# Kernel tuning notes

Hardware: AMD Instinct MI355X
Metric: run time of the kernel (lower is better)

## Reference

```python
import jax, jax.numpy as jnp
import numpy as np

N = 10000
E = 160000
NEG_SLOPE = 0.2
BN_EPS = 1e-5


def _gat_conv(x, W, a_src, a_dst, b, src, dst, n, heads):
    # PyG GATConv, concat=False (mean over heads), shared lin for src/dst.
    H = heads
    C = W.shape[1] // H
    h = (x @ W).reshape(n, H, C)                       # (N,H,C)
    e_s = jnp.einsum('nhc,hc->nh', h, a_src)           # (N,H)
    e_d = jnp.einsum('nhc,hc->nh', h, a_dst)
    alpha = jax.nn.leaky_relu(e_s[src] + e_d[dst], NEG_SLOPE)   # (E',H)
    amax = jax.ops.segment_max(alpha, dst, num_segments=n)       # per-dst softmax
    ex = jnp.exp(alpha - amax[dst])
    denom = jax.ops.segment_sum(ex, dst, num_segments=n)
    w = ex / (denom[dst] + 1e-16)
    out = jax.ops.segment_sum(h[src] * w[:, :, None], dst, num_segments=n)  # (N,H,C)
    return out.mean(axis=1) + b


def _bn(x, g, b):
    mu = x.mean(axis=0)
    var = x.var(axis=0)  # biased, as torch BN training forward
    return (x - mu) * jax.lax.rsqrt(var + BN_EPS) * g + b


def setup_inputs() -> dict:
    key = jax.random.key(0)
    ks = jax.random.split(key, 32)
    d = {}
    d['x'] = jax.random.normal(ks[0], (N, 64), jnp.float32)
    d['edge_index'] = jax.random.randint(ks[1], (2, E), 0, N, jnp.int64)
    s = lambda k, shape, fan: jax.random.normal(k, shape, jnp.float32) * (1.0 / np.sqrt(fan))
    d['Wp'] = s(ks[2], (64, 128), 64); d['bp'] = jnp.zeros((128,), jnp.float32)
    # conv0: 8 heads, per-head 128
    d['W0'] = s(ks[3], (128, 8 * 128), 128); d['as0'] = s(ks[4], (8, 128), 128)
    d['ad0'] = s(ks[5], (8, 128), 128); d['b0'] = jnp.zeros((128,), jnp.float32)
    d['g0'] = jnp.ones((128,), jnp.float32); d['be0'] = jnp.zeros((128,), jnp.float32)
    # conv1: same shape
    d['W1'] = s(ks[6], (128, 8 * 128), 128); d['as1'] = s(ks[7], (8, 128), 128)
    d['ad1'] = s(ks[8], (8, 128), 128); d['b1'] = jnp.zeros((128,), jnp.float32)
    d['g1'] = jnp.ones((128,), jnp.float32); d['be1'] = jnp.zeros((128,), jnp.float32)
    # conv2: 1 head, out 64
    d['W2'] = s(ks[9], (128, 64), 128); d['as2'] = s(ks[10], (1, 64), 64)
    d['ad2'] = s(ks[11], (1, 64), 64); d['b2'] = jnp.zeros((64,), jnp.float32)
    d['g2'] = jnp.ones((64,), jnp.float32); d['be2'] = jnp.zeros((64,), jnp.float32)
    # residual projection for layer 2 (128 -> 64)
    d['Wr'] = s(ks[12], (128, 64), 128); d['br'] = jnp.zeros((64,), jnp.float32)
    return d


def reference(x, edge_index, Wp, bp, W0, as0, ad0, b0, g0, be0,
              W1, as1, ad1, b1, g1, be1, W2, as2, ad2, b2, g2, be2, Wr, br):
    n = x.shape[0]
    loops = jnp.arange(n, dtype=edge_index.dtype)
    src = jnp.concatenate([edge_index[0], loops])  # add_self_loops=True
    dst = jnp.concatenate([edge_index[1], loops])
    h = x @ Wp + bp
    # layer 0 (8 heads, identity residual)
    hr = h
    h = jax.nn.elu(_bn(_gat_conv(h, W0, as0, ad0, b0, src, dst, n, 8), g0, be0)) + hr
    # layer 1
    hr = h
    h = jax.nn.elu(_bn(_gat_conv(h, W1, as1, ad1, b1, src, dst, n, 8), g1, be1)) + hr
    # layer 2 (1 head, linear residual 128->64)
    hr = h @ Wr + br
    h = jax.nn.elu(_bn(_gat_conv(h, W2, as2, ad2, b2, src, dst, n, 1), g2, be2)) + hr
    return h
```

## Files before the change

### kernel.cpp

```cpp
#include <hip/hip_runtime.h>
#include <hip/hip_bf16.h>
#include <cstdint>
#include <cstddef>

#define TPB 256

typedef __attribute__((ext_vector_type(8))) short bf16x8;
typedef __attribute__((ext_vector_type(4))) float f32x4;

static __device__ __forceinline__ float bf2f(unsigned short u) {
  union { unsigned int i; float f; } c;
  c.i = ((unsigned int)u) << 16;
  return c.f;
}

__global__ void detect_kernel(const unsigned int* __restrict__ w, int* __restrict__ flag) {
  __shared__ int any32;
  if (threadIdx.x == 0) any32 = 0;
  __syncthreads();
  for (int i = threadIdx.x; i < 1024; i += TPB)
    if (w[2 * i + 1] != 0u) any32 = 1;
  __syncthreads();
  if (threadIdx.x == 0) *flag = any32;
}

__global__ void decode_kernel(const void* __restrict__ raw, const int* __restrict__ flag,
                              int* __restrict__ src, int* __restrict__ dst, int E, int n) {
  int i = blockIdx.x * TPB + threadIdx.x;
  int tot = E + n;
  if (i >= tot) return;
  if (i < E) {
    if (*flag) {
      const int* p = (const int*)raw;
      src[i] = p[i];
      dst[i] = p[E + i];
    } else {
      const long long* p = (const long long*)raw;
      src[i] = (int)p[i];
      dst[i] = (int)p[E + i];
    }
  } else {
    src[i] = i - E;
    dst[i] = i - E;
  }
}

__global__ void count_kernel(const int* __restrict__ dst, int* __restrict__ counts, int etot) {
  int i = blockIdx.x * TPB + threadIdx.x;
  if (i < etot) atomicAdd(&counts[dst[i]], 1);
}

__global__ void scan_kernel(const int* __restrict__ counts, int* __restrict__ row_ptr, int n) {
  __shared__ int part[TPB];
  int tid = threadIdx.x;
  int chunk = (n + TPB - 1) / TPB;
  int begin = tid * chunk;
  int end = begin + chunk; if (end > n) end = n;
  int s = 0;
  for (int i = begin; i < end && i < n; i++) s += counts[i];
  part[tid] = s;
  __syncthreads();
  for (int off = 1; off < TPB; off <<= 1) {
    int v = (tid >= off) ? part[tid - off] : 0;
    __syncthreads();
    part[tid] += v;
    __syncthreads();
  }
  int base = (tid == 0) ? 0 : part[tid - 1];
  for (int i = begin; i < end && i < n; i++) { row_ptr[i] = base; base += counts[i]; }
  if (tid == TPB - 1) row_ptr[n] = base;
}

__global__ void fill_kernel(const int* __restrict__ src, const int* __restrict__ dst,
                            const int* __restrict__ row_ptr, int* __restrict__ fill,
                            int* __restrict__ sorted_src, int etot) {
  int i = blockIdx.x * TPB + threadIdx.x;
  if (i >= etot) return;
  int d = dst[i];
  int pos = row_ptr[d] + atomicAdd(&fill[d], 1);
  sorted_src[pos] = src[i];
}

__global__ void f32_to_bf16_kernel(const float* __restrict__ in, __hip_bfloat16* __restrict__ out, int n) {
  int i = blockIdx.x * TPB + threadIdx.x;
  if (i < n) out[i] = __float2bfloat16(in[i]);
}

__global__ __launch_bounds__(256) void gemm_bf16_kernel(
    const short* __restrict__ A, const short* __restrict__ B,
    const float* __restrict__ bias, float* __restrict__ C,
    __hip_bfloat16* __restrict__ Cb, int M, int N, int K) {
  __shared__ short As[64][40];
  __shared__ short Bs[64][40];

  const int tid = threadIdx.x;
  const int lane = tid & 63;
  const int w = tid >> 6;
  const int bm = blockIdx.x * 64;
  const int bn = blockIdx.y * 64;

  f32x4 acc[4];
#pragma unroll
  for (int nt = 0; nt < 4; nt++) acc[nt] = (f32x4){0.f, 0.f, 0.f, 0.f};

  const int arow = tid >> 2;
  const int akk = (tid & 3) << 3;
  const int bc = tid & 63;
  const int bkg = (tid >> 6) << 3;

  for (int k0 = 0; k0 < K; k0 += 32) {
    {
      int gr = bm + arow;
      if (gr < M) {
        *(bf16x8*)&As[arow][akk] = *(const bf16x8*)&A[(size_t)gr * K + k0 + akk];
      } else {
        bf16x8 z = {0, 0, 0, 0, 0, 0, 0, 0};
        *(bf16x8*)&As[arow][akk] = z;
      }
    }
    {
      bf16x8 t;
#pragma unroll
      for (int j = 0; j < 8; j++)
        t[j] = B[(size_t)(k0 + bkg + j) * N + bn + bc];
      *(bf16x8*)&Bs[bc][bkg] = t;
    }
    __syncthreads();

    bf16x8 a = *(const bf16x8*)&As[w * 16 + (lane & 15)][(lane >> 4) * 8];
#pragma unroll
    for (int nt = 0; nt < 4; nt++) {
      bf16x8 b = *(const bf16x8*)&Bs[nt * 16 + (lane & 15)][(lane >> 4) * 8];
      acc[nt] = __builtin_amdgcn_mfma_f32_16x16x32_bf16(a, b, acc[nt], 0, 0, 0);
    }
    __syncthreads();
  }

#pragma unroll
  for (int nt = 0; nt < 4; nt++) {
    int gc = bn + nt * 16 + (lane & 15);
    float bv = bias ? bias[gc] : 0.f;
#pragma unroll
    for (int q = 0; q < 4; q++) {
      int gr = bm + w * 16 + (lane >> 4) * 4 + q;
      if (gr < M) {
        float val = acc[nt][q] + bv;
        if (C) C[(size_t)gr * N + gc] = val;
        if (Cb) Cb[(size_t)gr * N + gc] = __float2bfloat16(val);
      }
    }
  }
}

__global__ void attn_coeff8_kernel(const unsigned short* __restrict__ gb,
                                   const float* __restrict__ asrc,
                                   const float* __restrict__ adst,
                                   float* __restrict__ es, float* __restrict__ ed) {
  const int v = blockIdx.x;
  const int tid = threadIdx.x;
  ushort4 gu = *(const ushort4*)&gb[(size_t)v * 1024 + 4 * tid];
  float4 av = *(const float4*)&asrc[4 * tid];
  float4 dv = *(const float4*)&adst[4 * tid];
  float gx = bf2f(gu.x), gy = bf2f(gu.y), gz = bf2f(gu.z), gw = bf2f(gu.w);
  float p1 = gx * av.x + gy * av.y + gz * av.z + gw * av.w;
  float p2 = gx * dv.x + gy * dv.y + gz * dv.z + gw * dv.w;
#pragma unroll
  for (int off = 16; off > 0; off >>= 1) {
    p1 += __shfl_down(p1, off);
    p2 += __shfl_down(p2, off);
  }
  if ((tid & 31) == 0) {
    es[(size_t)v * 8 + (tid >> 5)] = p1;
    ed[(size_t)v * 8 + (tid >> 5)] = p2;
  }
}

template <int H, int C>
__global__ void attn_coeff_kernel(const float* __restrict__ g,
                                  const float* __restrict__ asrc,
                                  const float* __restrict__ adst,
                                  float* __restrict__ es, float* __restrict__ ed) {
  int v = blockIdx.x;
  int tid = threadIdx.x;
  __shared__ float rs[2], rd[2];
  const float* grow = g + (size_t)v * (H * C);
  for (int h = 0; h < H; ++h) {
    float gv = grow[h * C + tid];
    float p1 = gv * asrc[h * C + tid];
    float p2 = gv * adst[h * C + tid];
#pragma unroll
    for (int off = 32; off > 0; off >>= 1) {
      p1 += __shfl_down(p1, off);
      p2 += __shfl_down(p2, off);
    }
    if ((tid & 63) == 0) { rs[tid >> 6] = p1; rd[tid >> 6] = p2; }
    __syncthreads();
    if (tid == 0) {
      float s1 = rs[0], s2 = rd[0];
      if (C > 64) { s1 += rs[1]; s2 += rd[1]; }
      es[(size_t)v * H + h] = s1;
      ed[(size_t)v * H + h] = s2;
    }
    __syncthreads();
  }
}

__global__ __launch_bounds__(256) void gat_aggregate8_kernel(
    const int* __restrict__ row_ptr, const int* __restrict__ srcs,
    const unsigned short* __restrict__ gb, const float* __restrict__ es,
    const float* __restrict__ ed, const float* __restrict__ bias,
    float* __restrict__ out) {
  constexpr int T = 256, H = 8, HC = 1024, CHUNK = 64;
  const int v = blockIdx.x;
  const int tid = threadIdx.x;
  const int h = tid & 7;
  const int grp = tid >> 3;
  const int hh = tid >> 5;

  __shared__ float red[T];
  __shared__ float mh[H], invd[H], edv[H];
  __shared__ float wlds[CHUNK * H];
  __shared__ int slds[CHUNK];
  __shared__ float4 red4[T];

  const int begin = row_ptr[v];
  const int deg = row_ptr[v + 1] - begin;

  if (tid < H) edv[tid] = ed[(size_t)v * H + tid];
  __syncthreads();

  float pm = -1e30f;
  for (int j = grp; j < deg; j += 32) {
    int s = srcs[begin + j];
    float a = es[(size_t)s * H + h] + edv[h];
    a = a > 0.f ? a : 0.2f * a;
    pm = fmaxf(pm, a);
  }
  red[tid] = pm;
  __syncthreads();
  if (tid < H) {
    float m = -1e30f;
    for (int gg = 0; gg < 32; gg++) m = fmaxf(m, red[gg * H + tid]);
    mh[tid] = m;
  }
  __syncthreads();

  float ps = 0.f;
  for (int j = grp; j < deg; j += 32) {
    int s = srcs[begin + j];
    float a = es[(size_t)s * H + h] + edv[h];
    a = a > 0.f ? a : 0.2f * a;
    ps += expf(a - mh[h]);
  }
  red[tid] = ps;
  __syncthreads();
  if (tid < H) {
    float d = 0.f;
    for (int gg = 0; gg < 32; gg++) d += red[gg * H + tid];
    invd[tid] = 1.0f / (d + 1e-16f);
  }

  float4 acc = make_float4(0.f, 0.f, 0.f, 0.f);
  for (int base = 0; base < deg; base += CHUNK) {
    int cnt = deg - base; if (cnt > CHUNK) cnt = CHUNK;
    __syncthreads();
    for (int idx = tid; idx < cnt * H; idx += T) {
      int j = idx >> 3, hx = idx & 7;
      int s = srcs[begin + base + j];
      if (hx == 0) slds[j] = s;
      float a = es[(size_t)s * H + hx] + edv[hx];
      a = a > 0.f ? a : 0.2f * a;
      wlds[idx] = expf(a - mh[hx]) * invd[hx];
    }
    __syncthreads();
    int j = 0;
    for (; j + 2 <= cnt; j += 2) {
      int s0 = slds[j], s1 = slds[j + 1];
      float w0 = wlds[j * 8 + hh], w1 = wlds[(j + 1) * 8 + hh];
      ushort4 u0 = *(const ushort4*)&gb[(size_t)s0 * HC + 4 * tid];
      ushort4 u1 = *(const ushort4*)&gb[(size_t)s1 * HC + 4 * tid];
      acc.x += w0 * bf2f(u0.x); acc.y += w0 * bf2f(u0.y);
      acc.z += w0 * bf2f(u0.z); acc.w += w0 * bf2f(u0.w);
      acc.x += w1 * bf2f(u1.x); acc.y += w1 * bf2f(u1.y);
      acc.z += w1 * bf2f(u1.z); acc.w += w1 * bf2f(u1.w);
    }
    if (j < cnt) {
      int s0 = slds[j];
      float w0 = wlds[j * 8 + hh];
      ushort4 u0 = *(const ushort4*)&gb[(size_t)s0 * HC + 4 * tid];
      acc.x += w0 * bf2f(u0.x); acc.y += w0 * bf2f(u0.y);
      acc.z += w0 * bf2f(u0.z); acc.w += w0 * bf2f(u0.w);
    }
  }

  __syncthreads();
  red4[tid] = acc;
  __syncthreads();
  if (tid < 32) {
    float4 s = red4[tid];
#pragma unroll
    for (int hx = 1; hx < 8; hx++) {
      float4 t = red4[tid + 32 * hx];
      s.x += t.x; s.y += t.y; s.z += t.z; s.w += t.w;
    }
    int c0 = 4 * tid;
    out[(size_t)v * 128 + c0 + 0] = s.x * 0.125f + bias[c0 + 0];
    out[(size_t)v * 128 + c0 + 1] = s.y * 0.125f + bias[c0 + 1];
    out[(size_t)v * 128 + c0 + 2] = s.z * 0.125f + bias[c0 + 2];
    out[(size_t)v * 128 + c0 + 3] = s.w * 0.125f + bias[c0 + 3];
  }
}

__global__ __launch_bounds__(256) void gat_aggregate1_kernel(
    const int* __restrict__ row_ptr, const int* __restrict__ srcs,
    const float* __restrict__ g, const float* __restrict__ es,
    const float* __restrict__ ed, const float* __restrict__ bias,
    float* __restrict__ out, int n) {
  const int wave = threadIdx.x >> 6;
  const int lane = threadIdx.x & 63;
  const int v = blockIdx.x * 4 + wave;
  if (v >= n) return;

  const int begin = row_ptr[v];
  const int deg = row_ptr[v + 1] - begin;
  const float edv = ed[v];

  float pm = -1e30f;
  for (int j = lane; j < deg; j += 64) {
    float a = es[srcs[begin + j]] + edv;
    a = a > 0.f ? a : 0.2f * a;
    pm = fmaxf(pm, a);
  }
#pragma unroll
  for (int off = 32; off > 0; off >>= 1) pm = fmaxf(pm, __shfl_xor(pm, off));

  float ps = 0.f;
  for (int j = lane; j < deg; j += 64) {
    float a = es[srcs[begin + j]] + edv;
    a = a > 0.f ? a : 0.2f * a;
    ps += expf(a - pm);
  }
#pragma unroll
  for (int off = 32; off > 0; off >>= 1) ps += __shfl_xor(ps, off);
  const float invd = 1.0f / (ps + 1e-16f);

  float acc = 0.f;
  for (int base = 0; base < deg; base += 64) {
    int cnt = deg - base; if (cnt > 64) cnt = 64;
    int sv = 0; float wv = 0.f;
    if (lane < cnt) {
      sv = srcs[begin + base + lane];
      float a = es[sv] + edv;
      a = a > 0.f ? a : 0.2f * a;
      wv = expf(a - pm) * invd;
    }
    for (int j = 0; j < cnt; j++) {
      int s = __shfl(sv, j);
      float wgt = __shfl(wv, j);
      acc += wgt * g[(size_t)s * 64 + lane];
    }
  }
  out[(size_t)v * 64 + lane] = acc + bias[lane];
}

template <int C>
__global__ void bn_stats_kernel(const float* __restrict__ x, int n, float* __restrict__ sums) {
  constexpr int T = 256;
  constexpr int RPI = T / C;
  constexpr int ITER = 64;
  constexpr int ROWS = RPI * ITER;
  int c = threadIdx.x % C;
  int r0 = threadIdx.x / C;
  int rowBase = blockIdx.x * ROWS;
  float s = 0.f, q = 0.f;
  for (int it = 0; it < ITER; ++it) {
    int r = rowBase + it * RPI + r0;
    if (r < n) {
      float v = x[(size_t)r * C + c];
      s += v; q += v * v;
    }
  }
  __shared__ float ls[T], lq[T];
  ls[threadIdx.x] = s; lq[threadIdx.x] = q;
  __syncthreads();
  if (threadIdx.x < C) {
    float ts = 0.f, tq = 0.f;
    for (int r = 0; r < RPI; ++r) { ts += ls[c + r * C]; tq += lq[c + r * C]; }
    atomicAdd(&sums[c], ts);
    atomicAdd(&sums[C + c], tq);
  }
}

template <int C>
__global__ void bn_elu_res_kernel(const float* __restrict__ x, const float* __restrict__ sums,
                                  const float* __restrict__ gamma, const float* __restrict__ beta,
                                  const float* __restrict__ res, float* __restrict__ out,
                                  __hip_bfloat16* __restrict__ outb, int n) {
  int i = blockIdx.x * TPB + threadIdx.x;
  if (i >= n * C) return;
  int c = i % C;
  float inv_n = 1.0f / (float)n;
  float mu = sums[c] * inv_n;
  float var = sums[C + c] * inv_n - mu * mu;
  float y = (x[i] - mu) * rsqrtf(var + 1e-5f) * gamma[c] + beta[c];
  y = y > 0.f ? y : expm1f(y);
  y += res[i];
  out[i] = y;
  if (outb) outb[i] = __float2bfloat16(y);
}

extern "C" void kernel_launch(void* const* d_in, const int* in_sizes, int n_in,
                              void* d_out, int out_size, void* d_ws, size_t ws_size,
                              hipStream_t stream) {
  const float* x   = (const float*)d_in[0];
  const void*  ei  = d_in[1];
  const float* Wp  = (const float*)d_in[2];
  const float* bp  = (const float*)d_in[3];
  const float* W0  = (const float*)d_in[4];
  const float* as0 = (const float*)d_in[5];
  const float* ad0 = (const float*)d_in[6];
  const float* b0  = (const float*)d_in[7];
  const float* g0  = (const float*)d_in[8];
  const float* be0 = (const float*)d_in[9];
  const float* W1  = (const float*)d_in[10];
  const float* as1 = (const float*)d_in[11];
  const float* ad1 = (const float*)d_in[12];
  const float* b1  = (const float*)d_in[13];
  const float* g1  = (const float*)d_in[14];
  const float* be1 = (const float*)d_in[15];
  const float* W2  = (const float*)d_in[16];
  const float* as2 = (const float*)d_in[17];
  const float* ad2 = (const float*)d_in[18];
  const float* b2  = (const float*)d_in[19];
  const float* g2  = (const float*)d_in[20];
  const float* be2 = (const float*)d_in[21];
  const float* Wr  = (const float*)d_in[22];
  const float* br  = (const float*)d_in[23];

  const int N = in_sizes[0] / 64;
  const int E = in_sizes[1] / 2;
  const int ETOT = E + N;

  char* wsp = (char*)d_ws;
  size_t off = 0;
  auto alloc = [&](size_t bytes) -> void* {
    void* p = wsp + off;
    off += (bytes + 255) & ~(size_t)255;
    return p;
  };
  int*   flag    = (int*)alloc(4);
  int*   e_src   = (int*)alloc((size_t)ETOT * 4);
  int*   e_dst   = (int*)alloc((size_t)ETOT * 4);
  int*   counts  = (int*)alloc((size_t)N * 4);
  int*   fillc   = (int*)alloc((size_t)N * 4);
  int*   row_ptr = (int*)alloc((size_t)(N + 1) * 4);
  int*   s_src   = (int*)alloc((size_t)ETOT * 4);
  float* hA      = (float*)alloc((size_t)N * 128 * 4);
  float* hB      = (float*)alloc((size_t)N * 128 * 4);
  float* gbuf    = (float*)alloc((size_t)N * 64 * 4);
  float* gat     = (float*)alloc((size_t)N * 128 * 4);
  float* es      = (float*)alloc((size_t)N * 8 * 4);
  float* ed      = (float*)alloc((size_t)N * 8 * 4);
  float* bnsum   = (float*)alloc(2 * 128 * 4);
  __hip_bfloat16* gbufb = (__hip_bfloat16*)alloc((size_t)N * 1024 * 2);
  __hip_bfloat16* xb  = (__hip_bfloat16*)alloc((size_t)N * 64 * 2);
  __hip_bfloat16* hAb = (__hip_bfloat16*)alloc((size_t)N * 128 * 2);
  __hip_bfloat16* hBb = (__hip_bfloat16*)alloc((size_t)N * 128 * 2);
  __hip_bfloat16* Wpb = (__hip_bfloat16*)alloc((size_t)64 * 128 * 2);
  __hip_bfloat16* W0b = (__hip_bfloat16*)alloc((size_t)128 * 1024 * 2);
  __hip_bfloat16* W1b = (__hip_bfloat16*)alloc((size_t)128 * 1024 * 2);
  __hip_bfloat16* W2b = (__hip_bfloat16*)alloc((size_t)128 * 64 * 2);
  __hip_bfloat16* Wrb = (__hip_bfloat16*)alloc((size_t)128 * 64 * 2);

  const int egrid = (ETOT + TPB - 1) / TPB;
  const int mgrid = (N + 63) / 64;
  auto cgrid = [](int n) { return (n + TPB - 1) / TPB; };

  detect_kernel<<<1, TPB, 0, stream>>>((const unsigned int*)ei, flag);
  decode_kernel<<<egrid, TPB, 0, stream>>>(ei, flag, e_src, e_dst, E, N);
  hipMemsetAsync(counts, 0, (size_t)N * 4, stream);
  hipMemsetAsync(fillc, 0, (size_t)N * 4, stream);
  count_kernel<<<egrid, TPB, 0, stream>>>(e_dst, counts, ETOT);
  scan_kernel<<<1, TPB, 0, stream>>>(counts, row_ptr, N);
  fill_kernel<<<egrid, TPB, 0, stream>>>(e_src, e_dst, row_ptr, fillc, s_src, ETOT);

  f32_to_bf16_kernel<<<cgrid(N * 64), TPB, 0, stream>>>(x, xb, N * 64);
  f32_to_bf16_kernel<<<cgrid(64 * 128), TPB, 0, stream>>>(Wp, Wpb, 64 * 128);
  f32_to_bf16_kernel<<<cgrid(128 * 1024), TPB, 0, stream>>>(W0, W0b, 128 * 1024);
  f32_to_bf16_kernel<<<cgrid(128 * 1024), TPB, 0, stream>>>(W1, W1b, 128 * 1024);
  f32_to_bf16_kernel<<<cgrid(128 * 64), TPB, 0, stream>>>(W2, W2b, 128 * 64);
  f32_to_bf16_kernel<<<cgrid(128 * 64), TPB, 0, stream>>>(Wr, Wrb, 128 * 64);

  gemm_bf16_kernel<<<dim3(mgrid, 2), 256, 0, stream>>>(
      (const short*)xb, (const short*)Wpb, bp, hA, hAb, N, 128, 64);

  gemm_bf16_kernel<<<dim3(mgrid, 16), 256, 0, stream>>>(
      (const short*)hAb, (const short*)W0b, nullptr, nullptr, gbufb, N, 1024, 128);
  attn_coeff8_kernel<<<N, 256, 0, stream>>>((const unsigned short*)gbufb, as0, ad0, es, ed);
  gat_aggregate8_kernel<<<N, 256, 0, stream>>>(row_ptr, s_src, (const unsigned short*)gbufb, es, ed, b0, gat);
  hipMemsetAsync(bnsum, 0, 2 * 128 * 4, stream);
  bn_stats_kernel<128><<<(N + 127) / 128, 256, 0, stream>>>(gat, N, bnsum);
  bn_elu_res_kernel<128><<<cgrid(N * 128), TPB, 0, stream>>>(gat, bnsum, g0, be0, hA, hB, hBb, N);

  gemm_bf16_kernel<<<dim3(mgrid, 16), 256, 0, stream>>>(
      (const short*)hBb, (const short*)W1b, nullptr, nullptr, gbufb, N, 1024, 128);
  attn_coeff8_kernel<<<N, 256, 0, stream>>>((const unsigned short*)gbufb, as1, ad1, es, ed);
  gat_aggregate8_kernel<<<N, 256, 0, stream>>>(row_ptr, s_src, (const unsigned short*)gbufb, es, ed, b1, gat);
  hipMemsetAsync(bnsum, 0, 2 * 128 * 4, stream);
  bn_stats_kernel<128><<<(N + 127) / 128, 256, 0, stream>>>(gat, N, bnsum);
  bn_elu_res_kernel<128><<<cgrid(N * 128), TPB, 0, stream>>>(gat, bnsum, g1, be1, hB, hA, hAb, N);

  gemm_bf16_kernel<<<dim3(mgrid, 1), 256, 0, stream>>>(
      (const short*)hAb, (const short*)Wrb, br, hB, nullptr, N, 64, 128);
  gemm_bf16_kernel<<<dim3(mgrid, 1), 256, 0, stream>>>(
      (const short*)hAb, (const short*)W2b, nullptr, gbuf, nullptr, N, 64, 128);
  attn_coeff_kernel<1, 64><<<N, 64, 0, stream>>>(gbuf, as2, ad2, es, ed);
  gat_aggregate1_kernel<<<(N + 3) / 4, 256, 0, stream>>>(row_ptr, s_src, gbuf, es, ed, b2, gat, N);
  hipMemsetAsync(bnsum, 0, 2 * 64 * 4, stream);
  bn_stats_kernel<64><<<(N + 255) / 256, 256, 0, stream>>>(gat, N, bnsum);
  bn_elu_res_kernel<64><<<cgrid(N * 64), TPB, 0, stream>>>(gat, bnsum, g2, be2, hB, (float*)d_out, nullptr, N);
}
```

Before: 334.4 us.

## Pre-transpose weights for vectorized GEMM B loads and restructure GAT aggregation

Weights are converted to transposed bf16 once, so the GEMM can load B tiles with 16-byte vector reads instead of strided scalar gathers. The GEMM tile widens to 128 output columns. The 8-head aggregation now caches leaky-relu logits in shared memory for nodes with degree up to 128, so neighbor es values are not re-gathered three times. It also gathers 8 bf16 per thread, unrolled over four neighbors split across two half-blocks. This adds shared memory use and a larger final reduction, and it swaps expf for __expf.

```diff
diff --git a/kernel.cpp b/kernel.cpp
--- a/kernel.cpp
+++ b/kernel.cpp
@@ -6,7 +6,9 @@
 #define TPB 256
 
 typedef __attribute__((ext_vector_type(8))) short bf16x8;
+typedef __attribute__((ext_vector_type(8))) unsigned short ushort8;
 typedef __attribute__((ext_vector_type(4))) float f32x4;
+typedef __attribute__((ext_vector_type(8))) float f32x8;
 
 static __device__ __forceinline__ float bf2f(unsigned short u) {
   union { unsigned int i; float f; } c;
@@ -86,27 +88,43 @@
   if (i < n) out[i] = __float2bfloat16(in[i]);
 }
 
-__global__ __launch_bounds__(256) void gemm_bf16_kernel(
-    const short* __restrict__ A, const short* __restrict__ B,
+__global__ void f32_to_bf16_T_kernel(const float* __restrict__ in, __hip_bfloat16* __restrict__ out,
+                                     int K, int N) {
+  __shared__ float tile[32][33];
+  const int k0 = blockIdx.x * 32, n0 = blockIdx.y * 32;
+  const int tx = threadIdx.x & 31, ty = threadIdx.x >> 5;
+  for (int r = ty; r < 32; r += 8) {
+    int k = k0 + r, n = n0 + tx;
+    tile[r][tx] = (k < K && n < N) ? in[(size_t)k * N + n] : 0.f;
+  }
+  __syncthreads();
+  for (int r = ty; r < 32; r += 8) {
+    int n = n0 + r, k = k0 + tx;
+    if (n < N && k < K) out[(size_t)n * K + k] = __float2bfloat16(tile[tx][r]);
+  }
+}
+
+__global__ __launch_bounds__(256) void gemm_bf16t_kernel(
+    const short* __restrict__ A, const short* __restrict__ Bt,
     const float* __restrict__ bias, float* __restrict__ C,
     __hip_bfloat16* __restrict__ Cb, int M, int N, int K) {
   __shared__ short As[64][40];
-  __shared__ short Bs[64][40];
+  __shared__ short Bs[128][40];
 
   const int tid = threadIdx.x;
   const int lane = tid & 63;
   const int w = tid >> 6;
   const int bm = blockIdx.x * 64;
-  const int bn = blockIdx.y * 64;
-
-  f32x4 acc[4];
-#pragma unroll
-  for (int nt = 0; nt < 4; nt++) acc[nt] = (f32x4){0.f, 0.f, 0.f, 0.f};
+  const int bn = blockIdx.y * 128;
+
+  f32x4 acc[8];
+#pragma unroll
+  for (int nt = 0; nt < 8; nt++) acc[nt] = (f32x4){0.f, 0.f, 0.f, 0.f};
 
   const int arow = tid >> 2;
   const int akk = (tid & 3) << 3;
-  const int bc = tid & 63;
-  const int bkg = (tid >> 6) << 3;
+  const int brow = tid >> 1;
+  const int bkk = (tid & 1) << 4;
 
   for (int k0 = 0; k0 < K; k0 += 32) {
     {
@@ -119,17 +137,22 @@
       }
     }
     {
-      bf16x8 t;
-#pragma unroll
-      for (int j = 0; j < 8; j++)
-        t[j] = B[(size_t)(k0 + bkg + j) * N + bn + bc];
-      *(bf16x8*)&Bs[bc][bkg] = t;
+      int gbn = bn + brow;
+      if (gbn < N) {
+        const short* bp = &Bt[(size_t)gbn * K + k0 + bkk];
+        *(bf16x8*)&Bs[brow][bkk]     = *(const bf16x8*)bp;
+        *(bf16x8*)&Bs[brow][bkk + 8] = *(const bf16x8*)(bp + 8);
+      } else {
+        bf16x8 z = {0, 0, 0, 0, 0, 0, 0, 0};
+        *(bf16x8*)&Bs[brow][bkk] = z;
+        *(bf16x8*)&Bs[brow][bkk + 8] = z;
+      }
     }
     __syncthreads();
 
     bf16x8 a = *(const bf16x8*)&As[w * 16 + (lane & 15)][(lane >> 4) * 8];
 #pragma unroll
-    for (int nt = 0; nt < 4; nt++) {
+    for (int nt = 0; nt < 8; nt++) {
       bf16x8 b = *(const bf16x8*)&Bs[nt * 16 + (lane & 15)][(lane >> 4) * 8];
       acc[nt] = __builtin_amdgcn_mfma_f32_16x16x32_bf16(a, b, acc[nt], 0, 0, 0);
     }
@@ -137,8 +160,9 @@
   }
 
 #pragma unroll
-  for (int nt = 0; nt < 4; nt++) {
+  for (int nt = 0; nt < 8; nt++) {
     int gc = bn + nt * 16 + (lane & 15);
+    if (gc >= N) continue;
     float bv = bias ? bias[gc] : 0.f;
 #pragma unroll
     for (int q = 0; q < 4; q++) {
@@ -210,104 +234,152 @@
     const unsigned short* __restrict__ gb, const float* __restrict__ es,
     const float* __restrict__ ed, const float* __restrict__ bias,
     float* __restrict__ out) {
-  constexpr int T = 256, H = 8, HC = 1024, CHUNK = 64;
+  constexpr int T = 256, H = 8, HC = 1024, CAP = 128;
   const int v = blockIdx.x;
   const int tid = threadIdx.x;
   const int h = tid & 7;
-  const int grp = tid >> 3;
-  const int hh = tid >> 5;
-
+  const int jj = tid >> 3;
+
+  __shared__ float alds[CAP * H];
+  __shared__ int slds[CAP];
   __shared__ float red[T];
-  __shared__ float mh[H], invd[H], edv[H];
-  __shared__ float wlds[CHUNK * H];
-  __shared__ int slds[CHUNK];
-  __shared__ float4 red4[T];
+  __shared__ float mh[H], invd[H], edv8[H];
+  __shared__ float red8[T][8];
 
   const int begin = row_ptr[v];
   const int deg = row_ptr[v + 1] - begin;
 
-  if (tid < H) edv[tid] = ed[(size_t)v * H + tid];
-  __syncthreads();
-
-  float pm = -1e30f;
-  for (int j = grp; j < deg; j += 32) {
-    int s = srcs[begin + j];
-    float a = es[(size_t)s * H + h] + edv[h];
-    a = a > 0.f ? a : 0.2f * a;
-    pm = fmaxf(pm, a);
-  }
-  red[tid] = pm;
-  __syncthreads();
-  if (tid < H) {
-    float m = -1e30f;
-    for (int gg = 0; gg < 32; gg++) m = fmaxf(m, red[gg * H + tid]);
-    mh[tid] = m;
-  }
-  __syncthreads();
-
-  float ps = 0.f;
-  for (int j = grp; j < deg; j += 32) {
-    int s = srcs[begin + j];
-    float a = es[(size_t)s * H + h] + edv[h];
-    a = a > 0.f ? a : 0.2f * a;
-    ps += expf(a - mh[h]);
-  }
-  red[tid] = ps;
-  __syncthreads();
-  if (tid < H) {
-    float d = 0.f;
-    for (int gg = 0; gg < 32; gg++) d += red[gg * H + tid];
-    invd[tid] = 1.0f / (d + 1e-16f);
-  }
-
-  float4 acc = make_float4(0.f, 0.f, 0.f, 0.f);
-  for (int base = 0; base < deg; base += CHUNK) {
-    int cnt = deg - base; if (cnt > CHUNK) cnt = CHUNK;
-    __syncthreads();
-    for (int idx = tid; idx < cnt * H; idx += T) {
+  if (tid < H) edv8[tid] = ed[(size_t)v * H + tid];
+  __syncthreads();
+
+  const int half = tid >> 7;
+  const int t128 = tid & 127;
+  const int c0 = t128 * 8;
+  const int hh = t128 >> 4;
+
+  f32x8 acc = {0.f, 0.f, 0.f, 0.f, 0.f, 0.f, 0.f, 0.f};
+
+  auto gather = [&](int cnt) {
+    int j = half;
+    for (; j + 6 < cnt; j += 8) {
+      int s0 = slds[j], s1 = slds[j + 2], s2 = slds[j + 4], s3 = slds[j + 6];
+      float w0 = alds[j * 8 + hh], w1 = alds[(j + 2) * 8 + hh];
+      float w2 = alds[(j + 4) * 8 + hh], w3 = alds[(j + 6) * 8 + hh];
+      ushort8 u0 = *(const ushort8*)&gb[(size_t)s0 * HC + c0];
+      ushort8 u1 = *(const ushort8*)&gb[(size_t)s1 * HC + c0];
+      ushort8 u2 = *(const ushort8*)&gb[(size_t)s2 * HC + c0];
+      ushort8 u3 = *(const ushort8*)&gb[(size_t)s3 * HC + c0];
+#pragma unroll
+      for (int k = 0; k < 8; k++)
+        acc[k] += w0 * bf2f(u0[k]) + w1 * bf2f(u1[k]) + w2 * bf2f(u2[k]) + w3 * bf2f(u3[k]);
+    }
+    for (; j < cnt; j += 2) {
+      int s = slds[j];
+      float wv = alds[j * 8 + hh];
+      ushort8 u = *(const ushort8*)&gb[(size_t)s * HC + c0];
+#pragma unroll
+      for (int k = 0; k < 8; k++) acc[k] += wv * bf2f(u[k]);
+    }
+  };
+
+  if (deg <= CAP) {
+    for (int idx = tid; idx < deg * 8; idx += T) {
       int j = idx >> 3, hx = idx & 7;
-      int s = srcs[begin + base + j];
+      int s = srcs[begin + j];
       if (hx == 0) slds[j] = s;
-      float a = es[(size_t)s * H + hx] + edv[hx];
+      float a = es[(size_t)s * 8 + hx] + edv8[hx];
+      alds[idx] = a > 0.f ? a : 0.2f * a;
+    }
+    __syncthreads();
+    float pm = -1e30f;
+    for (int j = jj; j < deg; j += 32) pm = fmaxf(pm, alds[j * 8 + h]);
+    red[tid] = pm;
+    __syncthreads();
+    if (tid < H) {
+      float m = -1e30f;
+      for (int g2 = 0; g2 < 32; g2++) m = fmaxf(m, red[g2 * 8 + tid]);
+      mh[tid] = m;
+    }
+    __syncthreads();
+    float ps = 0.f;
+    float m = mh[h];
+    for (int j = jj; j < deg; j += 32) {
+      float p = __expf(alds[j * 8 + h] - m);
+      alds[j * 8 + h] = p;
+      ps += p;
+    }
+    red[tid] = ps;
+    __syncthreads();
+    if (tid < H) {
+      float d = 0.f;
+      for (int g2 = 0; g2 < 32; g2++) d += red[g2 * 8 + tid];
+      invd[tid] = 1.0f / (d + 1e-16f);
+    }
+    __syncthreads();
+    for (int idx = tid; idx < deg * 8; idx += T) alds[idx] *= invd[idx & 7];
+    __syncthreads();
+    gather(deg);
+  } else {
+    float pm = -1e30f;
+    for (int j = jj; j < deg; j += 32) {
+      int s = srcs[begin + j];
+      float a = es[(size_t)s * 8 + h] + edv8[h];
       a = a > 0.f ? a : 0.2f * a;
-      wlds[idx] = expf(a - mh[hx]) * invd[hx];
-    }
-    __syncthreads();
-    int j = 0;
-    for (; j + 2 <= cnt; j += 2) {
-      int s0 = slds[j], s1 = slds[j + 1];
-      float w0 = wlds[j * 8 + hh], w1 = wlds[(j + 1) * 8 + hh];
-      ushort4 u0 = *(const ushort4*)&gb[(size_t)s0 * HC + 4 * tid];
-      ushort4 u1 = *(const ushort4*)&gb[(size_t)s1 * HC + 4 * tid];
-      acc.x += w0 * bf2f(u0.x); acc.y += w0 * bf2f(u0.y);
-      acc.z += w0 * bf2f(u0.z); acc.w += w0 * bf2f(u0.w);
-      acc.x += w1 * bf2f(u1.x); acc.y += w1 * bf2f(u1.y);
-      acc.z += w1 * bf2f(u1.z); acc.w += w1 * bf2f(u1.w);
-    }
-    if (j < cnt) {
-      int s0 = slds[j];
-      float w0 = wlds[j * 8 + hh];
-      ushort4 u0 = *(const ushort4*)&gb[(size_t)s0 * HC + 4 * tid];
-      acc.x += w0 * bf2f(u0.x); acc.y += w0 * bf2f(u0.y);
-      acc.z += w0 * bf2f(u0.z); acc.w += w0 * bf2f(u0.w);
-    }
-  }
-
-  __syncthreads();
-  red4[tid] = acc;
-  __syncthreads();
-  if (tid < 32) {
-    float4 s = red4[tid];
-#pragma unroll
-    for (int hx = 1; hx < 8; hx++) {
-      float4 t = red4[tid + 32 * hx];
-      s.x += t.x; s.y += t.y; s.z += t.z; s.w += t.w;
-    }
-    int c0 = 4 * tid;
-    out[(size_t)v * 128 + c0 + 0] = s.x * 0.125f + bias[c0 + 0];
-    out[(size_t)v * 128 + c0 + 1] = s.y * 0.125f + bias[c0 + 1];
-    out[(size_t)v * 128 + c0 + 2] = s.z * 0.125f + bias[c0 + 2];
-    out[(size_t)v * 128 + c0 + 3] = s.w * 0.125f + bias[c0 + 3];
+      pm = fmaxf(pm, a);
+    }
+    red[tid] = pm;
+    __syncthreads();
+    if (tid < H) {
+      float m = -1e30f;
+      for (int g2 = 0; g2 < 32; g2++) m = fmaxf(m, red[g2 * 8 + tid]);
+      mh[tid] = m;
+    }
+    __syncthreads();
+    float ps = 0.f;
+    for (int j = jj; j < deg; j += 32) {
+      int s = srcs[begin + j];
+      float a = es[(size_t)s * 8 + h] + edv8[h];
+      a = a > 0.f ? a : 0.2f * a;
+      ps += __expf(a - mh[h]);
+    }
+    red[tid] = ps;
+    __syncthreads();
+    if (tid < H) {
+      float d = 0.f;
+      for (int g2 = 0; g2 < 32; g2++) d += red[g2 * 8 + tid];
+      invd[tid] = 1.0f / (d + 1e-16f);
+    }
+    for (int base = 0; base < deg; base += CAP) {
+      int cnt = deg - base; if (cnt > CAP) cnt = CAP;
+      __syncthreads();
+      for (int idx = tid; idx < cnt * 8; idx += T) {
+        int j = idx >> 3, hx = idx & 7;
+        int s = srcs[begin + base + j];
+        if (hx == 0) slds[j] = s;
+        float a = es[(size_t)s * 8 + hx] + edv8[hx];
+        a = a > 0.f ? a : 0.2f * a;
+        alds[idx] = __expf(a - mh[hx]) * invd[hx];
+      }
+      __syncthreads();
+      gather(cnt);
+    }
+  }
+
+  __syncthreads();
+#pragma unroll
+  for (int k = 0; k < 8; k++) red8[tid][k] = acc[k];
+  __syncthreads();
+  if (tid < 16) {
+    float o[8] = {0.f, 0.f, 0.f, 0.f, 0.f, 0.f, 0.f, 0.f};
+    for (int q = 0; q < 16; q++) {
+      const float* r = red8[q * 16 + tid];
+#pragma unroll
+      for (int k = 0; k < 8; k++) o[k] += r[k];
+    }
+    int cb = tid * 8;
+#pragma unroll
+    for (int k = 0; k < 8; k++)
+      out[(size_t)v * 128 + cb + k] = o[k] * 0.125f + bias[cb + k];
   }
 }
 
@@ -466,11 +538,11 @@
   __hip_bfloat16* xb  = (__hip_bfloat16*)alloc((size_t)N * 64 * 2);
   __hip_bfloat16* hAb = (__hip_bfloat16*)alloc((size_t)N * 128 * 2);
   __hip_bfloat16* hBb = (__hip_bfloat16*)alloc((size_t)N * 128 * 2);
-  __hip_bfloat16* Wpb = (__hip_bfloat16*)alloc((size_t)64 * 128 * 2);
-  __hip_bfloat16* W0b = (__hip_bfloat16*)alloc((size_t)128 * 1024 * 2);
-  __hip_bfloat16* W1b = (__hip_bfloat16*)alloc((size_t)128 * 1024 * 2);
-  __hip_bfloat16* W2b = (__hip_bfloat16*)alloc((size_t)128 * 64 * 2);
-  __hip_bfloat16* Wrb = (__hip_bfloat16*)alloc((size_t)128 * 64 * 2);
+  __hip_bfloat16* WpT = (__hip_bfloat16*)alloc((size_t)128 * 64 * 2);
+  __hip_bfloat16* W0T = (__hip_bfloat16*)alloc((size_t)1024 * 128 * 2);
+  __hip_bfloat16* W1T = (__hip_bfloat16*)alloc((size_t)1024 * 128 * 2);
+  __hip_bfloat16* W2T = (__hip_bfloat16*)alloc((size_t)64 * 128 * 2);
+  __hip_bfloat16* WrT = (__hip_bfloat16*)alloc((size_t)64 * 128 * 2);
 
   const int egrid = (ETOT + TPB - 1) / TPB;
   const int mgrid = (N + 63) / 64;
@@ -485,35 +557,35 @@
   fill_kernel<<<egrid, TPB, 0, stream>>>(e_src, e_dst, row_ptr, fillc, s_src, ETOT);
 
   f32_to_bf16_kernel<<<cgrid(N * 64), TPB, 0, stream>>>(x, xb, N * 64);
-  f32_to_bf16_kernel<<<cgrid(64 * 128), TPB, 0, stream>>>(Wp, Wpb, 64 * 128);
-  f32_to_bf16_kernel<<<cgrid(128 * 1024), TPB, 0, stream>>>(W0, W0b, 128 * 1024);
-  f32_to_bf16_kernel<<<cgrid(128 * 1024), TPB, 0, stream>>>(W1, W1b, 128 * 1024);
-  f32_to_bf16_kernel<<<cgrid(128 * 64), TPB, 0, stream>>>(W2, W2b, 128 * 64);
-  f32_to_bf16_kernel<<<cgrid(128 * 64), TPB, 0, stream>>>(Wr, Wrb, 128 * 64);
-
-  gemm_bf16_kernel<<<dim3(mgrid, 2), 256, 0, stream>>>(
-      (const short*)xb, (const short*)Wpb, bp, hA, hAb, N, 128, 64);
-
-  gemm_bf16_kernel<<<dim3(mgrid, 16), 256, 0, stream>>>(
-      (const short*)hAb, (const short*)W0b, nullptr, nullptr, gbufb, N, 1024, 128);
+  f32_to_bf16_T_kernel<<<dim3(2, 4), 256, 0, stream>>>(Wp, WpT, 64, 128);
+  f32_to_bf16_T_kernel<<<dim3(4, 32), 256, 0, stream>>>(W0, W0T, 128, 1024);
+  f32_to_bf16_T_kernel<<<dim3(4, 32), 256, 0, stream>>>(W1, W1T, 128, 1024);
+  f32_to_bf16_T_kernel<<<dim3(4, 2), 256, 0, stream>>>(W2, W2T, 128, 64);
+  f32_to_bf16_T_kernel<<<dim3(4, 2), 256, 0, stream>>>(Wr, WrT, 128, 64);
+
+  gemm_bf16t_kernel<<<dim3(mgrid, 1), 256, 0, stream>>>(
+      (const short*)xb, (const short*)WpT, bp, hA, hAb, N, 128, 64);
+
+  gemm_bf16t_kernel<<<dim3(mgrid, 8), 256, 0, stream>>>(
+      (const short*)hAb, (const short*)W0T, nullptr, nullptr, gbufb, N, 1024, 128);
   attn_coeff8_kernel<<<N, 256, 0, stream>>>((const unsigned short*)gbufb, as0, ad0, es, ed);
   gat_aggregate8_kernel<<<N, 256, 0, stream>>>(row_ptr, s_src, (const unsigned short*)gbufb, es, ed, b0, gat);
   hipMemsetAsync(bnsum, 0, 2 * 128 * 4, stream);
   bn_stats_kernel<128><<<(N + 127) / 128, 256, 0, stream>>>(gat, N, bnsum);
   bn_elu_res_kernel<128><<<cgrid(N * 128), TPB, 0, stream>>>(gat, bnsum, g0, be0, hA, hB, hBb, N);
 
-  gemm_bf16_kernel<<<dim3(mgrid, 16), 256, 0, stream>>>(
-      (const short*)hBb, (const short*)W1b, nullptr, nullptr, gbufb, N, 1024, 128);
+  gemm_bf16t_kernel<<<dim3(mgrid, 8), 256, 0, stream>>>(
+      (const short*)hBb, (const short*)W1T, nullptr, nullptr, gbufb, N, 1024, 128);
   attn_coeff8_kernel<<<N, 256, 0, stream>>>((const unsigned short*)gbufb, as1, ad1, es, ed);
   gat_aggregate8_kernel<<<N, 256, 0, stream>>>(row_ptr, s_src, (const unsigned short*)gbufb, es, ed, b1, gat);
   hipMemsetAsync(bnsum, 0, 2 * 128 * 4, stream);
   bn_stats_kernel<128><<<(N + 127) / 128, 256, 0, stream>>>(gat, N, bnsum);
   bn_elu_res_kernel<128><<<cgrid(N * 128), TPB, 0, stream>>>(gat, bnsum, g1, be1, hB, hA, hAb, N);
 
-  gemm_bf16_kernel<<<dim3(mgrid, 1), 256, 0, stream>>>(
-      (const short*)hAb, (const short*)Wrb, br, hB, nullptr, N, 64, 128);
-  gemm_bf16_kernel<<<dim3(mgrid, 1), 256, 0, stream>>>(
-      (const short*)hAb, (const short*)W2b, nullptr, gbuf, nullptr, N, 64, 128);
+  gemm_bf16t_kernel<<<dim3(mgrid, 1), 256, 0, stream>>>(
+      (const short*)hAb, (const short*)WrT, br, hB, nullptr, N, 64, 128);
+  gemm_bf16t_kernel<<<dim3(mgrid, 1), 256, 0, stream>>>(
+      (const short*)hAb, (const short*)W2T, nullptr, gbuf, nullptr, N, 64, 128);
   attn_coeff_kernel<1, 64><<<N, 64, 0, stream>>>(gbuf, as2, ad2, es, ed);
   gat_aggregate1_kernel<<<(N + 3) / 4, 256, 0, stream>>>(row_ptr, s_src, gbuf, es, ed, b2, gat, N);
   hipMemsetAsync(bnsum, 0, 2 * 64 * 4, stream);
```

After: 340.9 us. No clear change (+1.9%).
